# Kernel optimization log

Measured on AMD Instinct MI355X. Metric: run time of the kernel, lower is better.

Reference implementation:

```python
import jax, jax.numpy as jnp
import numpy as np

CODE_SIZE = 8
NUM_HEADS = 16
KC = 2 ** CODE_SIZE  # 256 codebook buckets


def setup_inputs() -> dict:
    key = jax.random.key(0)
    ks = jax.random.split(key, 6)
    B, Lq, Lk, C = 8, 2048, 4096, 1024
    q = jax.random.normal(ks[0], (B * Lq, C), jnp.float32)
    k = jax.random.normal(ks[1], (B * Lk, C), jnp.float32)
    v = jax.random.normal(ks[2], (B * Lk, C), jnp.float32)
    Wc = jax.random.normal(ks[3], (CODE_SIZE, C), jnp.float32) * (C ** -0.5)  # code_proj weight
    bc = jnp.zeros((CODE_SIZE,), jnp.float32)                                  # code_proj bias
    codebook = jax.random.normal(ks[4], (2 * CODE_SIZE, C), jnp.float32) * 0.02
    lengths = jnp.full((B,), Lk, jnp.int32)      # kv tokens per sample
    inv_lengths = jnp.full((B,), Lq, jnp.int32)  # q tokens per sample
    return dict(q=q, k=k, v=v, Wc=Wc, bc=bc, codebook=codebook,
                lengths=lengths, inv_lengths=inv_lengths)


def reference(q, k, v, Wc, bc, codebook, lengths, inv_lengths):
    C = q.shape[-1]
    d = C // NUM_HEADS
    scale = d ** -0.5
    B = lengths.shape[0]
    Lk = k.shape[0] // B  # equal per-sample kv lengths
    Lq = q.shape[0] // B  # equal per-sample q lengths

    # --- binary spherical quantization of k ---
    code = k @ Wc.T + bc
    code = code / jnp.linalg.norm(code, axis=-1, keepdims=True)
    # sign in {-1,+1}/sqrt(cs); affine *sqrt(cs)/2 + 0.5 -> bits in {0,1}
    bits = (code >= 0).astype(jnp.int32)                      # [B*Lk, cs]
    code_base = 2 ** jnp.arange(CODE_SIZE - 1, -1, -1)        # [cs]
    idxs = (bits * code_base).sum(-1)                         # [B*Lk] in [0, 256)

    # --- dense codebook keys for all 2^cs codes ---
    base_bits = (jnp.arange(KC)[:, None] // code_base) % 2    # [K, cs]
    base = jnp.concatenate([base_bits, 1 - base_bits], axis=-1).astype(codebook.dtype)  # [K, 2cs]
    cod_k = base @ codebook                                   # [K, C]

    # --- scatter-add v and counts into per-sample buckets ---
    b_idx = jnp.repeat(jnp.arange(B), Lk)                     # batch id per kv token
    flat = b_idx * KC + idxs                                  # [B*Lk]
    cod_v = jax.ops.segment_sum(v, flat, num_segments=B * KC).reshape(B, KC, C)
    counts = jax.ops.segment_sum(jnp.ones((B * Lk,), q.dtype), flat,
                                 num_segments=B * KC).reshape(B, KC)

    # --- bucketed attention with quotient normalization ---
    qh = q.reshape(B, Lq, NUM_HEADS, d)
    kh = cod_k.reshape(KC, NUM_HEADS, d)
    vh = cod_v.reshape(B, KC, NUM_HEADS, d)
    scores = scale * jnp.einsum('blhd,khd->blhk', qh, kh)     # [B,Lq,H,K]
    bias = jnp.where(counts > 0, 0.0, -jnp.inf)[:, None, None, :]  # mask empty buckets
    attn = jax.nn.softmax(scores + bias, axis=-1)
    num = jnp.einsum('blhk,bkhd->blhd', attn, vh)             # attn @ summed-v
    den = jnp.einsum('blhk,bk->blh', attn, counts)            # attn @ counts
    out = num / den[..., None]
    return out.reshape(B * Lq, C)
```

## Files before the change

### kernel.cpp

```cpp
#include <hip/hip_runtime.h>
#include <hip/hip_bf16.h>

constexpr int B  = 8;
constexpr int LQ = 2048;
constexpr int LK = 4096;
constexpr int C  = 1024;
constexpr int H  = 16;
constexpr int D  = 64;
constexpr int CS = 8;
constexpr int KC = 256;
constexpr float SCALE = 0.125f;

typedef __attribute__((ext_vector_type(8))) short short8;
typedef __attribute__((ext_vector_type(4))) float f32x4;

union FragU { unsigned u[4]; short8 s; float4 f; };

__device__ inline unsigned bfp(float a, float b) {
  float2 f2; f2.x = a; f2.y = b;
  __hip_bfloat162 h = __float22bfloat162_rn(f2);
  return *reinterpret_cast<unsigned*>(&h);
}
__device__ inline unsigned short bf1(float a) {
  __hip_bfloat16 h = __float2bfloat16(a);
  return *reinterpret_cast<unsigned short*>(&h);
}

__global__ __launch_bounds__(256) void k_codes(
    const float* __restrict__ kmat, const float* __restrict__ Wc,
    const float* __restrict__ bc, int* __restrict__ idx)
{
  __shared__ float wS[CS * C];
  const int tid = threadIdx.x;
  {
    const float4* wsrc = (const float4*)Wc;
    float4* wdst = (float4*)wS;
#pragma unroll
    for (int i = 0; i < 8; ++i) wdst[tid + i * 256] = wsrc[tid + i * 256];
  }
  float bcr[CS];
#pragma unroll
  for (int j = 0; j < CS; ++j) bcr[j] = bc[j];
  __syncthreads();

  const int wave = tid >> 6, lane = tid & 63;

  for (int i = 0; i < 8; ++i) {
    const int r = blockIdx.x * 32 + wave * 8 + i;
    const float4* krow = (const float4*)(kmat + (size_t)r * C);
    float acc[CS];
#pragma unroll
    for (int j = 0; j < CS; ++j) acc[j] = 0.f;
#pragma unroll
    for (int rep = 0; rep < 4; ++rep) {
      float4 kv = krow[rep * 64 + lane];
      const int dbase = (rep * 64 + lane) * 4;
#pragma unroll
      for (int j = 0; j < CS; ++j) {
        float4 wv = *(const float4*)&wS[j * C + dbase];
        acc[j] += kv.x * wv.x + kv.y * wv.y + kv.z * wv.z + kv.w * wv.w;
      }
    }
#pragma unroll
    for (int j = 0; j < CS; ++j) {
#pragma unroll
      for (int off = 32; off >= 1; off >>= 1)
        acc[j] += __shfl_xor(acc[j], off, 64);
    }
    if (lane == 0) {
      int ix = 0;
#pragma unroll
      for (int j = 0; j < CS; ++j)
        ix |= ((acc[j] + bcr[j]) >= 0.f ? 1 : 0) << (7 - j);
      idx[r] = ix;
    }
  }
}

__global__ __launch_bounds__(256) void k_sort(
    const int* __restrict__ idx, int* __restrict__ offs,
    int* __restrict__ cnti, int* __restrict__ perm,
    float4* __restrict__ vfc)
{
  __shared__ int idxS[LK];
  __shared__ int hist[KC];
  __shared__ int cur[KC];
  __shared__ int wsum[4];
  const int b = blockIdx.x, t = threadIdx.x;
  const int lane = t & 63, w = t >> 6;

  hist[t] = 0;
  __syncthreads();
  for (int i = t; i < LK; i += 256) {
    const int ix = idx[b * LK + i];
    idxS[i] = ix;
    atomicAdd(&hist[ix], 1);
  }
  __syncthreads();

  const int myc = hist[t];
  int scan = myc;
#pragma unroll
  for (int off = 1; off < 64; off <<= 1) {
    int u = __shfl_up(scan, off, 64);
    if (lane >= off) scan += u;
  }
  if (lane == 63) wsum[w] = scan;
  __syncthreads();
  int base = 0;
#pragma unroll
  for (int i = 0; i < 4; ++i) base += (i < w) ? wsum[i] : 0;
  const int start = b * LK + base + scan - myc;
  offs[b * KC + t] = start;
  cnti[b * KC + t] = myc;
  cur[t] = start;
  __syncthreads();

  for (int i = t; i < LK; i += 256) {
    const int pos = atomicAdd(&cur[idxS[i]], 1);
    perm[pos] = b * LK + i;
  }

  for (int i = t; i < 512; i += 256) {
    const int qc = i >> 6, ln = i & 63;
    FragU u4;
    if ((ln & 15) == 0) {
      const int* cs = hist + (qc * 4 + (ln >> 4)) * 8;
      u4.u[0] = bfp((float)cs[0], (float)cs[1]);
      u4.u[1] = bfp((float)cs[2], (float)cs[3]);
      u4.u[2] = bfp((float)cs[4], (float)cs[5]);
      u4.u[3] = bfp((float)cs[6], (float)cs[7]);
    } else {
      u4.u[0] = u4.u[1] = u4.u[2] = u4.u[3] = 0u;
    }
    vfc[b * 512 + i] = u4.f;
  }
}

__global__ __launch_bounds__(256) void k_gather(
    const float* __restrict__ v, const int* __restrict__ perm,
    const int* __restrict__ offs, const int* __restrict__ cnti,
    unsigned short* __restrict__ vbf)
{
  __shared__ int permS[512];
  const int t = threadIdx.x;
  const int ix = blockIdx.x, b = blockIdx.y;
  const int start = offs[b * KC + ix];
  const int cnt = cnti[b * KC + ix];

  float4 acc = make_float4(0.f, 0.f, 0.f, 0.f);
  for (int base = 0; base < cnt; base += 512) {
    const int n = min(512, cnt - base);
    __syncthreads();
    for (int i = t; i < n; i += 256) permS[i] = perm[start + base + i];
    __syncthreads();
    int i = 0;
    for (; i + 4 <= n; i += 4) {
      const int r0 = permS[i], r1 = permS[i + 1];
      const int r2 = permS[i + 2], r3 = permS[i + 3];
      float4 a = *(const float4*)(v + (size_t)r0 * C + t * 4);
      float4 b4 = *(const float4*)(v + (size_t)r1 * C + t * 4);
      float4 c4 = *(const float4*)(v + (size_t)r2 * C + t * 4);
      float4 d4 = *(const float4*)(v + (size_t)r3 * C + t * 4);
      acc.x += a.x + b4.x + c4.x + d4.x;
      acc.y += a.y + b4.y + c4.y + d4.y;
      acc.z += a.z + b4.z + c4.z + d4.z;
      acc.w += a.w + b4.w + c4.w + d4.w;
    }
    for (; i < n; ++i) {
      const int r0 = permS[i];
      float4 a = *(const float4*)(v + (size_t)r0 * C + t * 4);
      acc.x += a.x; acc.y += a.y; acc.z += a.z; acc.w += a.w;
    }
  }

  const int h = t >> 4;
  const int n0 = (t & 15) * 4;
  const int o = ix >> 3, r = ix & 7;
  const int slot0 = ((o >> 2) * 4 + (n0 >> 4)) * 64 + (o & 3) * 16 + (n0 & 15);
  unsigned short* dst = vbf + ((size_t)((b * 16 + h) * 2048 + slot0)) * 8 + r;
  dst[0]  = bf1(acc.x);
  dst[8]  = bf1(acc.y);
  dst[16] = bf1(acc.z);
  dst[24] = bf1(acc.w);
}

__global__ __launch_bounds__(256) void k_attn(
    const float* __restrict__ q, const float* __restrict__ cb,
    const float4* __restrict__ vfb, const float4* __restrict__ vfc,
    float* __restrict__ out)
{
  __shared__ __align__(16) char smem[18432];
  float4* QA  = (float4*)smem;
  float4* CBf = (float4*)(smem + 16384);
  float*  TS  = (float*)smem;

  const int tid = threadIdx.x;
  const int lane = tid & 63, wq = tid >> 6, quad = lane >> 4;
  const int h = blockIdx.y, b = blockIdx.z;
  const int q0 = blockIdx.x * 128;

#pragma unroll
  for (int it = 0; it < 4; ++it) {
    const int od = tid & 7, m = it * 32 + (tid >> 3);
    const float* src = q + (size_t)(b * LQ + q0 + m) * C + h * D + od * 8;
    float4 f0 = *(const float4*)src, f1 = *(const float4*)(src + 4);
    FragU u;
    u.u[0] = bfp(f0.x * SCALE, f0.y * SCALE);
    u.u[1] = bfp(f0.z * SCALE, f0.w * SCALE);
    u.u[2] = bfp(f1.x * SCALE, f1.y * SCALE);
    u.u[3] = bfp(f1.z * SCALE, f1.w * SCALE);
    QA[((m >> 4) * 2 + (od >> 2)) * 64 + (od & 3) * 16 + (m & 15)] = u.f;
  }
  if (tid < 128) {
    const int od = tid & 7, j = tid >> 3;
    const float* src = cb + (size_t)j * C + h * D + od * 8;
    float4 f0 = *(const float4*)src, f1 = *(const float4*)(src + 4);
    FragU u;
    u.u[0] = bfp(f0.x, f0.y); u.u[1] = bfp(f0.z, f0.w);
    u.u[2] = bfp(f1.x, f1.y); u.u[3] = bfp(f1.z, f1.w);
    CBf[(od >> 2) * 64 + (od & 3) * 16 + j] = u.f;
  }
  __syncthreads();

  f32x4 tacc[2];
#pragma unroll
  for (int mt2 = 0; mt2 < 2; ++mt2) {
    const int mt = wq * 2 + mt2;
    FragU a0, a1, b0, b1;
    a0.f = QA[(mt * 2 + 0) * 64 + lane];
    a1.f = QA[(mt * 2 + 1) * 64 + lane];
    b0.f = CBf[0 * 64 + lane];
    b1.f = CBf[1 * 64 + lane];
    f32x4 z = {0.f, 0.f, 0.f, 0.f};
    z = __builtin_amdgcn_mfma_f32_16x16x32_bf16(a0.s, b0.s, z, 0, 0, 0);
    z = __builtin_amdgcn_mfma_f32_16x16x32_bf16(a1.s, b1.s, z, 0, 0, 0);
    tacc[mt2] = z;
  }
  __syncthreads();

#pragma unroll
  for (int mt2 = 0; mt2 < 2; ++mt2) {
    const int mt = wq * 2 + mt2;
#pragma unroll
    for (int r = 0; r < 4; ++r)
      TS[mt * 272 + (quad * 4 + r) * 17 + (lane & 15)] = tacc[mt2][r];
  }
  float t0[16], t1[16];
#pragma unroll
  for (int j = 0; j < 16; ++j) {
    t0[j] = TS[(wq * 2 + 0) * 272 + (lane & 15) * 17 + j];
    t1[j] = TS[(wq * 2 + 1) * 272 + (lane & 15) * 17 + j];
  }

  float esl0[8], esl1[8];
#pragma unroll
  for (int c = 0; c < 8; ++c) {
    esl0[c] = __expf(((c & 4) ? t0[5] : t0[13]) + ((c & 2) ? t0[6] : t0[14]) +
                     ((c & 1) ? t0[7] : t0[15]));
    esl1[c] = __expf(((c & 4) ? t1[5] : t1[13]) + ((c & 2) ? t1[6] : t1[14]) +
                     ((c & 1) ? t1[7] : t1[15]));
  }

  f32x4 acc[2][5];
#pragma unroll
  for (int i = 0; i < 2; ++i)
#pragma unroll
    for (int t_ = 0; t_ < 5; ++t_) acc[i][t_] = (f32x4){0.f, 0.f, 0.f, 0.f};

  const float4* vb = vfb + (size_t)(b * 16 + h) * 2048 + lane;
  const float4* vc = vfc + b * 512 + lane;

#pragma unroll
  for (int qc = 0; qc < 8; ++qc) {
    FragU bf0, bf1_, bf2, bf3, cf;
    bf0.f = vb[(qc * 4 + 0) * 64];
    bf1_.f = vb[(qc * 4 + 1) * 64];
    bf2.f = vb[(qc * 4 + 2) * 64];
    bf3.f = vb[(qc * 4 + 3) * 64];
    cf.f  = vc[qc * 64];

    const int u = qc * 4 + quad;
    const float eshi0 = __expf(
        ((u & 16) ? t0[0] : t0[8]) + ((u & 8) ? t0[1] : t0[9]) +
        ((u & 4) ? t0[2] : t0[10]) + ((u & 2) ? t0[3] : t0[11]) +
        ((u & 1) ? t0[4] : t0[12]));
    const float eshi1 = __expf(
        ((u & 16) ? t1[0] : t1[8]) + ((u & 8) ? t1[1] : t1[9]) +
        ((u & 4) ? t1[2] : t1[10]) + ((u & 2) ? t1[3] : t1[11]) +
        ((u & 1) ? t1[4] : t1[12]));

    FragU a0, a1;
    a0.u[0] = bfp(eshi0 * esl0[0], eshi0 * esl0[1]);
    a0.u[1] = bfp(eshi0 * esl0[2], eshi0 * esl0[3]);
    a0.u[2] = bfp(eshi0 * esl0[4], eshi0 * esl0[5]);
    a0.u[3] = bfp(eshi0 * esl0[6], eshi0 * esl0[7]);
    a1.u[0] = bfp(eshi1 * esl1[0], eshi1 * esl1[1]);
    a1.u[1] = bfp(eshi1 * esl1[2], eshi1 * esl1[3]);
    a1.u[2] = bfp(eshi1 * esl1[4], eshi1 * esl1[5]);
    a1.u[3] = bfp(eshi1 * esl1[6], eshi1 * esl1[7]);

    acc[0][0] = __builtin_amdgcn_mfma_f32_16x16x32_bf16(a0.s, bf0.s,  acc[0][0], 0, 0, 0);
    acc[1][0] = __builtin_amdgcn_mfma_f32_16x16x32_bf16(a1.s, bf0.s,  acc[1][0], 0, 0, 0);
    acc[0][1] = __builtin_amdgcn_mfma_f32_16x16x32_bf16(a0.s, bf1_.s, acc[0][1], 0, 0, 0);
    acc[1][1] = __builtin_amdgcn_mfma_f32_16x16x32_bf16(a1.s, bf1_.s, acc[1][1], 0, 0, 0);
    acc[0][2] = __builtin_amdgcn_mfma_f32_16x16x32_bf16(a0.s, bf2.s,  acc[0][2], 0, 0, 0);
    acc[1][2] = __builtin_amdgcn_mfma_f32_16x16x32_bf16(a1.s, bf2.s,  acc[1][2], 0, 0, 0);
    acc[0][3] = __builtin_amdgcn_mfma_f32_16x16x32_bf16(a0.s, bf3.s,  acc[0][3], 0, 0, 0);
    acc[1][3] = __builtin_amdgcn_mfma_f32_16x16x32_bf16(a1.s, bf3.s,  acc[1][3], 0, 0, 0);
    acc[0][4] = __builtin_amdgcn_mfma_f32_16x16x32_bf16(a0.s, cf.s,   acc[0][4], 0, 0, 0);
    acc[1][4] = __builtin_amdgcn_mfma_f32_16x16x32_bf16(a1.s, cf.s,   acc[1][4], 0, 0, 0);
  }

  const int srcl = lane & 48;
#pragma unroll
  for (int mt2 = 0; mt2 < 2; ++mt2) {
#pragma unroll
    for (int r = 0; r < 4; ++r) {
      const float den = __shfl(acc[mt2][4][r], srcl, 64);
      const float inv = 1.0f / den;
      const int row = q0 + wq * 32 + mt2 * 16 + quad * 4 + r;
      float* op = out + (size_t)(b * LQ + row) * C + h * D + (lane & 15);
#pragma unroll
      for (int t_ = 0; t_ < 4; ++t_) op[t_ * 16] = acc[mt2][t_][r] * inv;
    }
  }
}

extern "C" void kernel_launch(void* const* d_in, const int* in_sizes, int n_in,
                              void* d_out, int out_size, void* d_ws, size_t ws_size,
                              hipStream_t stream) {
  (void)in_sizes; (void)n_in; (void)out_size; (void)ws_size;
  const float* q  = (const float*)d_in[0];
  const float* k  = (const float*)d_in[1];
  const float* v  = (const float*)d_in[2];
  const float* Wc = (const float*)d_in[3];
  const float* bc = (const float*)d_in[4];
  const float* cb = (const float*)d_in[5];
  float* out = (float*)d_out;

  char* ws = (char*)d_ws;
  int*    idxp  = (int*)ws;
  int*    offsp = (int*)(ws + 0x20000);
  int*    cntip = (int*)(ws + 0x22000);
  int*    permp = (int*)(ws + 0x24000);
  float4* vfcp  = (float4*)(ws + 0x44000);
  unsigned short* vbfp = (unsigned short*)(ws + 0x60000);

  hipLaunchKernelGGL(k_codes, dim3(1024), dim3(256), 0, stream,
                     k, Wc, bc, idxp);
  hipLaunchKernelGGL(k_sort, dim3(B), dim3(256), 0, stream,
                     idxp, offsp, cntip, permp, vfcp);
  hipLaunchKernelGGL(k_gather, dim3(KC, B), dim3(256), 0, stream,
                     v, permp, offsp, cntip, vbfp);
  hipLaunchKernelGGL(k_attn, dim3(LQ / 128, H, B), dim3(256), 0, stream,
                     q, cb, (const float4*)vbfp, (const float4*)vfcp, out);
}
```

Baseline: 376.9 us.

## Split gather writeback into coalesced repack kernel, widen sort, swizzle attn blocks

The gather kernel now writes packed bf16 pairs contiguously into a temporary buffer, and a new repack kernel transposes them through shared memory into the MFMA fragment layout. This replaces the scattered 2-byte stores the gather kernel used before. The sort kernel runs with 1024 threads per block so the histogram and permutation loops take fewer iterations. The attention kernel remaps block indices to change the scheduling order and writes its output with nontemporal stores. The cost is an extra kernel launch and an extra round trip through the workspace.

After: 375.3 us. No clear change (-0.4%).

```diff
diff --git a/kernel.cpp b/kernel.cpp
--- a/kernel.cpp
+++ b/kernel.cpp
@@ -21,10 +21,6 @@
   __hip_bfloat162 h = __float22bfloat162_rn(f2);
   return *reinterpret_cast<unsigned*>(&h);
 }
-__device__ inline unsigned short bf1(float a) {
-  __hip_bfloat16 h = __float2bfloat16(a);
-  return *reinterpret_cast<unsigned short*>(&h);
-}
 
 __global__ __launch_bounds__(256) void k_codes(
     const float* __restrict__ kmat, const float* __restrict__ Wc,
@@ -77,7 +73,7 @@
   }
 }
 
-__global__ __launch_bounds__(256) void k_sort(
+__global__ __launch_bounds__(1024) void k_sort(
     const int* __restrict__ idx, int* __restrict__ offs,
     int* __restrict__ cnti, int* __restrict__ perm,
     float4* __restrict__ vfc)
@@ -89,40 +85,45 @@
   const int b = blockIdx.x, t = threadIdx.x;
   const int lane = t & 63, w = t >> 6;
 
-  hist[t] = 0;
-  __syncthreads();
-  for (int i = t; i < LK; i += 256) {
+  if (t < KC) hist[t] = 0;
+  __syncthreads();
+  for (int i = t; i < LK; i += 1024) {
     const int ix = idx[b * LK + i];
     idxS[i] = ix;
     atomicAdd(&hist[ix], 1);
   }
   __syncthreads();
 
-  const int myc = hist[t];
-  int scan = myc;
-#pragma unroll
-  for (int off = 1; off < 64; off <<= 1) {
-    int u = __shfl_up(scan, off, 64);
-    if (lane >= off) scan += u;
-  }
-  if (lane == 63) wsum[w] = scan;
-  __syncthreads();
-  int base = 0;
-#pragma unroll
-  for (int i = 0; i < 4; ++i) base += (i < w) ? wsum[i] : 0;
-  const int start = b * LK + base + scan - myc;
-  offs[b * KC + t] = start;
-  cnti[b * KC + t] = myc;
-  cur[t] = start;
-  __syncthreads();
-
-  for (int i = t; i < LK; i += 256) {
+  int myc = 0, scan = 0;
+  if (t < KC) {
+    myc = hist[t];
+    scan = myc;
+#pragma unroll
+    for (int off = 1; off < 64; off <<= 1) {
+      int u = __shfl_up(scan, off, 64);
+      if (lane >= off) scan += u;
+    }
+    if (lane == 63) wsum[w] = scan;
+  }
+  __syncthreads();
+  if (t < KC) {
+    int base = 0;
+#pragma unroll
+    for (int i = 0; i < 4; ++i) base += (i < w) ? wsum[i] : 0;
+    const int start = b * LK + base + scan - myc;
+    offs[b * KC + t] = start;
+    cnti[b * KC + t] = myc;
+    cur[t] = start;
+  }
+  __syncthreads();
+
+  for (int i = t; i < LK; i += 1024) {
     const int pos = atomicAdd(&cur[idxS[i]], 1);
     perm[pos] = b * LK + i;
   }
 
-  for (int i = t; i < 512; i += 256) {
-    const int qc = i >> 6, ln = i & 63;
+  if (t < 512) {
+    const int qc = t >> 6, ln = t & 63;
     FragU u4;
     if ((ln & 15) == 0) {
       const int* cs = hist + (qc * 4 + (ln >> 4)) * 8;
@@ -133,14 +134,14 @@
     } else {
       u4.u[0] = u4.u[1] = u4.u[2] = u4.u[3] = 0u;
     }
-    vfc[b * 512 + i] = u4.f;
+    vfc[b * 512 + t] = u4.f;
   }
 }
 
 __global__ __launch_bounds__(256) void k_gather(
     const float* __restrict__ v, const int* __restrict__ perm,
     const int* __restrict__ offs, const int* __restrict__ cnti,
-    unsigned short* __restrict__ vbf)
+    unsigned* __restrict__ vtmp)
 {
   __shared__ int permS[512];
   const int t = threadIdx.x;
@@ -174,15 +175,41 @@
     }
   }
 
-  const int h = t >> 4;
-  const int n0 = (t & 15) * 4;
-  const int o = ix >> 3, r = ix & 7;
-  const int slot0 = ((o >> 2) * 4 + (n0 >> 4)) * 64 + (o & 3) * 16 + (n0 & 15);
-  unsigned short* dst = vbf + ((size_t)((b * 16 + h) * 2048 + slot0)) * 8 + r;
-  dst[0]  = bf1(acc.x);
-  dst[8]  = bf1(acc.y);
-  dst[16] = bf1(acc.z);
-  dst[24] = bf1(acc.w);
+  uint2 wv;
+  wv.x = bfp(acc.x, acc.y);
+  wv.y = bfp(acc.z, acc.w);
+  *((uint2*)(vtmp + (((size_t)(b * KC + ix)) << 9)) + t) = wv;
+}
+
+__global__ __launch_bounds__(256) void k_repack(
+    const unsigned* __restrict__ vtmp, float4* __restrict__ vfb)
+{
+  __shared__ unsigned U[8][522];
+  const int o = blockIdx.x, b = blockIdx.y, t = threadIdx.x;
+  for (int i = t; i < 8 * 512; i += 256) {
+    const int j = i >> 9, c = i & 511;
+    U[j][c] = vtmp[(((size_t)(b * KC + o * 8 + j)) << 9) + c];
+  }
+  __syncthreads();
+#pragma unroll
+  for (int pp = 0; pp < 2; ++pp) {
+    const int p = t + pp * 256;
+    const int h = p >> 5;
+    const int n = (2 * p) & 63;
+    const int s = ((o >> 2) * 4 + (n >> 4)) * 64 + (o & 3) * 16 + (n & 15);
+    unsigned Ur[8];
+#pragma unroll
+    for (int j = 0; j < 8; ++j) Ur[j] = U[j][p];
+    FragU lo, hi;
+#pragma unroll
+    for (int j = 0; j < 4; ++j) {
+      lo.u[j] = (Ur[2 * j] & 0xffffu) | (Ur[2 * j + 1] << 16);
+      hi.u[j] = (Ur[2 * j] >> 16) | (Ur[2 * j + 1] & 0xffff0000u);
+    }
+    float4* outp = vfb + (size_t)(b * 16 + h) * 2048 + s;
+    outp[0] = lo.f;
+    outp[1] = hi.f;
+  }
 }
 
 __global__ __launch_bounds__(256) void k_attn(
@@ -197,8 +224,12 @@
 
   const int tid = threadIdx.x;
   const int lane = tid & 63, wq = tid >> 6, quad = lane >> 4;
-  const int h = blockIdx.y, b = blockIdx.z;
-  const int q0 = blockIdx.x * 128;
+
+  const int lin = blockIdx.x + 16 * blockIdx.y + 256 * blockIdx.z;
+  const int ns = (lin & 7) * 256 + (lin >> 3);
+  const int q0 = (ns & 15) * 128;
+  const int h = (ns >> 4) & 15;
+  const int b = ns >> 8;
 
 #pragma unroll
   for (int it = 0; it < 4; ++it) {
@@ -322,7 +353,8 @@
       const int row = q0 + wq * 32 + mt2 * 16 + quad * 4 + r;
       float* op = out + (size_t)(b * LQ + row) * C + h * D + (lane & 15);
 #pragma unroll
-      for (int t_ = 0; t_ < 4; ++t_) op[t_ * 16] = acc[mt2][t_][r] * inv;
+      for (int t_ = 0; t_ < 4; ++t_)
+        __builtin_nontemporal_store(acc[mt2][t_][r] * inv, op + t_ * 16);
     }
   }
 }
@@ -346,13 +378,16 @@
   int*    permp = (int*)(ws + 0x24000);
   float4* vfcp  = (float4*)(ws + 0x44000);
   unsigned short* vbfp = (unsigned short*)(ws + 0x60000);
+  unsigned* vtmpp = (unsigned*)(ws + 0x460000);
 
   hipLaunchKernelGGL(k_codes, dim3(1024), dim3(256), 0, stream,
                      k, Wc, bc, idxp);
-  hipLaunchKernelGGL(k_sort, dim3(B), dim3(256), 0, stream,
+  hipLaunchKernelGGL(k_sort, dim3(B), dim3(1024), 0, stream,
                      idxp, offsp, cntip, permp, vfcp);
   hipLaunchKernelGGL(k_gather, dim3(KC, B), dim3(256), 0, stream,
-                     v, permp, offsp, cntip, vbfp);
+                     v, permp, offsp, cntip, vtmpp);
+  hipLaunchKernelGGL(k_repack, dim3(32, B), dim3(256), 0, stream,
+                     vtmpp, (float4*)vbfp);
   hipLaunchKernelGGL(k_attn, dim3(LQ / 128, H, B), dim3(256), 0, stream,
                      q, cb, (const float4*)vbfp, (const float4*)vfcp, out);
 }
```
